# Optimization experiments

Hardware: AMD Instinct MI355X
Metric: run time of the kernel (lower is better)

Reference implementation:

```python
import jax, jax.numpy as jnp
import numpy as np

B, C, H, W = 16, 256, 112, 112
WS = 7           # window size
DH = 64          # dim_head
NH = C // DH     # num heads
EPS = 1e-5       # BatchNorm eps


def setup_inputs() -> dict:
    key = jax.random.key(0)
    ks = jax.random.split(key, 12)
    s = lambda k, shape, sc=0.05: jax.random.normal(k, shape, dtype=jnp.float32) * sc
    return dict(
        x_edge=jax.random.normal(ks[0], (B, C, H, W), dtype=jnp.float32),
        x_vit=jax.random.normal(ks[1], (B, C, H, W), dtype=jnp.float32),
        bn1_g=jnp.ones((C,), jnp.float32), bn1_b=jnp.zeros((C,), jnp.float32),
        bn1_m=s(ks[2], (C,)), bn1_v=jnp.abs(s(ks[3], (C,))) + 1.0,
        wq=s(ks[4], (C, C)), wk=s(ks[5], (C, C)), wv=s(ks[6], (C, C)),
        dw_w=s(ks[7], (C, 1, 3, 3)),
        bn2_g=jnp.ones((C,), jnp.float32), bn2_b=jnp.zeros((C,), jnp.float32),
        bn2_m=s(ks[8], (C,)), bn2_v=jnp.abs(s(ks[9], (C,))) + 1.0,
        eca_w=s(ks[10], (1, 1, 3)),
        wp=s(ks[11], (C, C)),
    )


def _bn(x, g, b, m, v):
    # eval-mode BatchNorm2d on NCHW
    scale = g * jax.lax.rsqrt(v + EPS)
    return (x - m[:, None, None]) * scale[:, None, None] + b[:, None, None]


def reference(x_edge, x_vit, bn1_g, bn1_b, bn1_m, bn1_v, wq, wk, wv, dw_w,
              bn2_g, bn2_b, bn2_m, bn2_v, eca_w, wp):
    x_fused = _bn(x_vit + x_edge, bn1_g, bn1_b, bn1_m, bn1_v)
    nh, nw = H // WS, W // WS  # H,W multiples of WS -> no padding needed

    def unfold(x):  # (B,C,H,W) -> (B*nh*nw, C, ws, ws)
        x = x.reshape(B, C, nh, WS, nw, WS).transpose(0, 2, 4, 1, 3, 5)
        return x.reshape(B * nh * nw, C, WS, WS)

    qw, kw, vw = unfold(x_edge), unfold(x_vit), unfold(x_fused)

    def heads(y):  # (N,C,ws,ws) -> (N, NH, ws*ws, DH)
        return y.reshape(-1, NH, DH, WS * WS).transpose(0, 1, 3, 2)

    q = heads(jnp.einsum('oc,ncij->noij', wq, qw))
    k = heads(jnp.einsum('oc,ncij->noij', wk, kw))
    v = heads(jax.nn.relu(jnp.einsum('oc,ncij->noij', wv, vw)))

    attn = jax.nn.softmax(jnp.einsum('nhqd,nhkd->nhqk', q, k) * (DH ** -0.5), axis=-1)
    x_sp = jnp.einsum('nhqk,nhkd->nhqd', attn, v)
    x_sp = x_sp.transpose(0, 1, 3, 2).reshape(-1, C, WS, WS)

    # importance-weighted blend with v_windows
    imp = jnp.abs(attn).mean(axis=(-1, -2)).mean(axis=1)  # (N,)
    imp = imp / (imp.max() + 1e-6)
    imp = imp[:, None, None, None]
    x_sp = imp * x_sp + (1.0 - imp) * vw

    # fold windows back to (B,C,H,W)
    x = x_sp.reshape(B, nh, nw, C, WS, WS).transpose(0, 3, 1, 4, 2, 5).reshape(B, C, H, W)

    # conv_local: depthwise 3x3 -> BN -> SiLU
    y = jax.lax.conv_general_dilated(x, dw_w, (1, 1), [(1, 1), (1, 1)],
                                     dimension_numbers=('NCHW', 'OIHW', 'NCHW'),
                                     feature_group_count=C)
    y = jax.nn.silu(_bn(y, bn2_g, bn2_b, bn2_m, bn2_v))

    # ECA: global avg pool -> conv1d over channels -> sigmoid gate
    p = y.mean(axis=(2, 3))[:, None, :]  # (B,1,C)
    a = jax.lax.conv_general_dilated(p, eca_w, (1,), [(1, 1)],
                                     dimension_numbers=('NCH', 'OIH', 'NCH'))
    y = y * jax.nn.sigmoid(a)[:, 0, :, None, None]

    # output 1x1 projection + skip
    y = jnp.einsum('oc,bcij->boij', wp, y)
    return x + y
```

## Files before the change

kernel.cpp:

```cpp
#include <hip/hip_runtime.h>

typedef unsigned short u16;
typedef __bf16 bf16x4 __attribute__((ext_vector_type(4)));
typedef __bf16 bf16x8 __attribute__((ext_vector_type(8)));
typedef float f32x4 __attribute__((ext_vector_type(4)));

#define MFMA_BF16(a, b, c) __builtin_amdgcn_mfma_f32_16x16x32_bf16((a), (b), (c), 0, 0, 0)
#define COMPILER_FENCE() asm volatile("" ::: "memory")

__device__ __forceinline__ bf16x8 ld_g16(const __bf16* p) {
  return *(const bf16x8*)p;
}
__device__ __forceinline__ bf16x8 ld_s16(const void* base, int byteoff) {
  return *(const bf16x8*)((const char*)base + byteoff);
}

__device__ __forceinline__ void proj_mfma(const __bf16* __restrict__ Wg,
                                          const __bf16* src, f32x4 (&acc)[4][4],
                                          int w, int lm, int lg)
{
  for (int ks = 0; ks < 8; ++ks) {
    bf16x8 afr[4], bfr[4];
#pragma unroll
    for (int mt = 0; mt < 4; ++mt)
      afr[mt] = ld_g16(Wg + (w * 64 + mt * 16 + lm) * 256 + ks * 32 + lg * 8);
#pragma unroll
    for (int nt = 0; nt < 4; ++nt) {
      int p = nt * 16 + lm;
      bfr[nt] = ld_s16(src, p * 512 + (((ks * 32 + lg * 8) * 2) ^ ((p & 7) << 4)));
    }
    __builtin_amdgcn_s_setprio(1);
#pragma unroll
    for (int mt = 0; mt < 4; ++mt)
#pragma unroll
      for (int nt = 0; nt < 4; ++nt)
        acc[mt][nt] = MFMA_BF16(afr[mt], bfr[nt], acc[mt][nt]);
    __builtin_amdgcn_s_setprio(0);
  }
}

__global__ void k0_setup(const float* __restrict__ wq, const float* __restrict__ wk,
                         const float* __restrict__ wv, const float* __restrict__ wp,
                         const float* __restrict__ g1, const float* __restrict__ b1,
                         const float* __restrict__ m1, const float* __restrict__ v1,
                         const float* __restrict__ g2, const float* __restrict__ b2,
                         const float* __restrict__ m2, const float* __restrict__ v2,
                         __bf16* __restrict__ wqb, __bf16* __restrict__ wkb,
                         __bf16* __restrict__ wvb, __bf16* __restrict__ wpb,
                         float* __restrict__ betav,
                         float* __restrict__ s2o, float* __restrict__ b2o)
{
  const int t = threadIdx.x;
  const int i = blockIdx.x * 256 + t;
  const int c = t;
  float s1 = g1[c] * rsqrtf(v1[c] + 1e-5f);
  wqb[i] = (__bf16)wq[i];
  wkb[i] = (__bf16)wk[i];
  wvb[i] = (__bf16)(wv[i] * s1);
  wpb[i] = (__bf16)wp[i];
  float contrib = wv[i] * (b1[c] - m1[c] * s1);
  contrib += __shfl_xor(contrib, 1);
  contrib += __shfl_xor(contrib, 2);
  contrib += __shfl_xor(contrib, 4);
  contrib += __shfl_xor(contrib, 8);
  contrib += __shfl_xor(contrib, 16);
  contrib += __shfl_xor(contrib, 32);
  __shared__ float rb[4];
  if ((t & 63) == 0) rb[t >> 6] = contrib;
  __syncthreads();
  if (t == 0) betav[blockIdx.x] = rb[0] + rb[1] + rb[2] + rb[3];
  if (blockIdx.x == 0) {
    float s2 = g2[t] * rsqrtf(v2[t] + 1e-5f);
    s2o[t] = s2;
    b2o[t] = b2[t] - m2[t] * s2;
  }
}

__global__ __launch_bounds__(256, 3) void k_pre(
    const float* __restrict__ xe, const float* __restrict__ xv,
    __bf16* __restrict__ tiles, int hb)
{
  __shared__ __align__(16) __bf16 st[32][788];
  const int t = threadIdx.x;
  const int blk = blockIdx.x;
  const int cg = blk & 7;
  const int wh = (blk >> 3) & 15;
  const int bl = blk >> 7;
  const int b = hb + bl;
  const int c0 = cg * 32;

  for (int s = 0; s < 2; ++s) {
    const float* src = (s == 0 ? xe : xv) + ((size_t)(b * 256 + c0) * 112 + wh * 7) * 112;
    for (int i = t; i < 6272; i += 256) {
      int cc = i / 196;
      int rem = i - cc * 196;
      f32x4 v = *(const f32x4*)(src + cc * 12544 + rem * 4);
      bf16x4 bv;
#pragma unroll
      for (int j = 0; j < 4; ++j) bv[j] = (__bf16)v[j];
      *(bf16x4*)&st[cc][rem * 4] = bv;
    }
    __syncthreads();
    for (int j = t; j < 3136; j += 256) {
      int row = j >> 2, sub = j & 3;
      int ww = row / 49, p = row - ww * 49;
      int y = p / 7, x = ww * 7 + (p - y * 7);
      int cs = sub * 8;
      bf16x8 v;
#pragma unroll
      for (int q = 0; q < 8; ++q) v[q] = st[cs + q][y * 112 + x];
      int n = (bl * 16 + wh) * 16 + ww;
      size_t off = (size_t)n * 50176 + s * 25088 + p * 512
                 + (((c0 + cs) * 2) ^ ((p & 7) << 4));
      *(bf16x8*)((char*)tiles + off) = v;
    }
    __syncthreads();
  }
}

__global__ __launch_bounds__(512, 4) void k1_attn(
    const __bf16* __restrict__ tiles,
    const __bf16* __restrict__ wqb, const __bf16* __restrict__ wkb,
    const __bf16* __restrict__ wvb, const float* __restrict__ betav,
    float* __restrict__ xout, int hb)
{
  __shared__ __align__(16) __bf16 B0[16384];
  __shared__ __align__(16) __bf16 B1[16384];

  const int t = threadIdx.x;
  const int n = blockIdx.x;
  const int bl = n >> 8, wh = (n >> 4) & 15, ww = n & 15;
  const int b = hb + bl;
  const int y0 = wh * 7, x0 = ww * 7;

  for (int idx = t; idx < 15 * 256; idx += 512) {
    int off = (49 + (idx >> 8)) * 512 + (idx & 255) * 2;
    *(__bf16*)((char*)B0 + off) = (__bf16)0.f;
    *(__bf16*)((char*)B1 + off) = (__bf16)0.f;
  }
  {
    const char* tb = (const char*)tiles + (size_t)n * 50176;
    for (int j = t; j < 3136; j += 512) {
      bf16x8 v = *(const bf16x8*)(tb + j * 16);
      char* d = (j < 1568) ? ((char*)B0 + j * 16) : ((char*)B1 + (j - 1568) * 16);
      *(bf16x8*)d = v;
    }
  }
  __syncthreads();

  const int w = t >> 6;
  const int l = t & 63;
  const int lm = l & 15, lg = l >> 4;
  const int h = w >> 1;
  const int half = w & 1;
  const int ob = w * 32;

  f32x4 vac[2][4] = {};
  {
    f32x4 qac[2][4] = {};
    for (int ks = 0; ks < 8; ++ks) {
      bf16x8 aq[2], av[2], bf[4];
#pragma unroll
      for (int mt = 0; mt < 2; ++mt) {
        int row = (ob + mt * 16 + lm) * 256 + ks * 32 + lg * 8;
        aq[mt] = ld_g16(wqb + row);
        av[mt] = ld_g16(wvb + row);
      }
#pragma unroll
      for (int nt = 0; nt < 4; ++nt) {
        int p = nt * 16 + lm;
        bf[nt] = ld_s16(B0, p * 512 + (((ks * 32 + lg * 8) * 2) ^ ((p & 7) << 4)));
      }
      __builtin_amdgcn_s_setprio(1);
#pragma unroll
      for (int mt = 0; mt < 2; ++mt)
#pragma unroll
        for (int nt = 0; nt < 4; ++nt) {
          qac[mt][nt] = MFMA_BF16(aq[mt], bf[nt], qac[mt][nt]);
          vac[mt][nt] = MFMA_BF16(av[mt], bf[nt], vac[mt][nt]);
        }
      __builtin_amdgcn_s_setprio(0);
    }
    __syncthreads();
#pragma unroll
    for (int mt = 0; mt < 2; ++mt)
#pragma unroll
      for (int nt = 0; nt < 4; ++nt) {
        int o0 = ob + mt * 16 + lg * 4;
        int p = nt * 16 + lm;
        bf16x4 v4;
#pragma unroll
        for (int r = 0; r < 4; ++r) v4[r] = (__bf16)qac[mt][nt][r];
        *(bf16x4*)((char*)B0 + p * 512 + ((o0 * 2) ^ ((p & 7) << 4))) = v4;
      }
  }

  {
    f32x4 kac[2][4] = {};
    for (int ks = 0; ks < 8; ++ks) {
      bf16x8 ak[2], av[2], bf[4];
#pragma unroll
      for (int mt = 0; mt < 2; ++mt) {
        int row = (ob + mt * 16 + lm) * 256 + ks * 32 + lg * 8;
        ak[mt] = ld_g16(wkb + row);
        av[mt] = ld_g16(wvb + row);
      }
#pragma unroll
      for (int nt = 0; nt < 4; ++nt) {
        int p = nt * 16 + lm;
        bf[nt] = ld_s16(B1, p * 512 + (((ks * 32 + lg * 8) * 2) ^ ((p & 7) << 4)));
      }
      __builtin_amdgcn_s_setprio(1);
#pragma unroll
      for (int mt = 0; mt < 2; ++mt)
#pragma unroll
        for (int nt = 0; nt < 4; ++nt) {
          kac[mt][nt] = MFMA_BF16(ak[mt], bf[nt], kac[mt][nt]);
          vac[mt][nt] = MFMA_BF16(av[mt], bf[nt], vac[mt][nt]);
        }
      __builtin_amdgcn_s_setprio(0);
    }
    __syncthreads();
#pragma unroll
    for (int mt = 0; mt < 2; ++mt)
#pragma unroll
      for (int nt = 0; nt < 4; ++nt) {
        int o0 = ob + mt * 16 + lg * 4;
        int p = nt * 16 + lm;
        bf16x4 v4;
#pragma unroll
        for (int r = 0; r < 4; ++r) v4[r] = (__bf16)kac[mt][nt][r];
        *(bf16x4*)((char*)B1 + p * 512 + ((o0 * 2) ^ ((p & 7) << 4))) = v4;
      }
  }
  __syncthreads();

  f32x4 sacc[2][4] = {};
  for (int ks = 0; ks < 2; ++ks) {
    bf16x8 aq[2], bk[4];
#pragma unroll
    for (int mt = 0; mt < 2; ++mt) {
      int qp = half * 32 + mt * 16 + lm;
      aq[mt] = ld_s16(B0, qp * 512 + (((h * 64 + ks * 32 + lg * 8) * 2) ^ ((qp & 7) << 4)));
    }
#pragma unroll
    for (int nt = 0; nt < 4; ++nt) {
      int kp = nt * 16 + lm;
      bk[nt] = ld_s16(B1, kp * 512 + (((h * 64 + ks * 32 + lg * 8) * 2) ^ ((kp & 7) << 4)));
    }
    __builtin_amdgcn_s_setprio(1);
#pragma unroll
    for (int mt = 0; mt < 2; ++mt)
#pragma unroll
      for (int nt = 0; nt < 4; ++nt)
        sacc[mt][nt] = MFMA_BF16(bk[nt], aq[mt], sacc[mt][nt]);
    __builtin_amdgcn_s_setprio(0);
  }

  COMPILER_FENCE();
#pragma unroll
  for (int mt = 0; mt < 2; ++mt) {
    float mx = -3.0e38f;
#pragma unroll
    for (int nt = 0; nt < 4; ++nt)
#pragma unroll
      for (int r = 0; r < 4; ++r) {
        float s = sacc[mt][nt][r] * 0.125f;
        sacc[mt][nt][r] = s;
        bool valid = (nt < 3) || (lg == 0 && r == 0);
        if (valid) mx = fmaxf(mx, s);
      }
    mx = fmaxf(mx, __shfl_xor(mx, 16));
    mx = fmaxf(mx, __shfl_xor(mx, 32));
    float sum = 0.f;
#pragma unroll
    for (int nt = 0; nt < 4; ++nt)
#pragma unroll
      for (int r = 0; r < 4; ++r) {
        bool valid = (nt < 3) || (lg == 0 && r == 0);
        float e = valid ? __expf(sacc[mt][nt][r] - mx) : 0.f;
        sacc[mt][nt][r] = e;
        sum += e;
      }
    sum += __shfl_xor(sum, 16);
    sum += __shfl_xor(sum, 32);
    float inv = 1.f / sum;
    int qp = half * 32 + mt * 16 + lm;
    int rowb = qp * 512 + h * 128;
    int sw = (qp & 7) << 4;
#pragma unroll
    for (int nt = 0; nt < 4; ++nt) {
      bf16x4 v4;
#pragma unroll
      for (int r = 0; r < 4; ++r) v4[r] = (__bf16)(sacc[mt][nt][r] * inv);
      int kp0 = nt * 16 + lg * 4;
      *(bf16x4*)((char*)B0 + rowb + ((kp0 * 2) ^ sw)) = v4;
    }
  }
  __syncthreads();

  {
    float beta[2][4];
#pragma unroll
    for (int mt = 0; mt < 2; ++mt) {
      f32x4 bv = *(const f32x4*)(betav + ob + mt * 16 + lg * 4);
#pragma unroll
      for (int r = 0; r < 4; ++r) beta[mt][r] = bv[r];
    }
#pragma unroll
    for (int mt = 0; mt < 2; ++mt)
#pragma unroll
      for (int nt = 0; nt < 4; ++nt)
#pragma unroll
        for (int r = 0; r < 4; ++r) {
          int o = ob + mt * 16 + lg * 4 + r;
          int kp = nt * 16 + lm;
          float val = fmaxf(vac[mt][nt][r] + beta[mt][r], 0.f);
          int off = o * 128 + ((kp * 2) ^ ((o & 7) << 4));
          *(__bf16*)((char*)B1 + off) = (__bf16)val;
        }
  }
  __syncthreads();

  f32x4 oacc[4][2] = {};
  for (int ks = 0; ks < 2; ++ks) {
    bf16x8 pf[2], bv[4];
#pragma unroll
    for (int mt = 0; mt < 2; ++mt) {
      int qp = half * 32 + mt * 16 + lm;
      pf[mt] = ld_s16(B0, qp * 512 + h * 128 + (((ks * 32 + lg * 8) * 2) ^ ((qp & 7) << 4)));
    }
#pragma unroll
    for (int nt = 0; nt < 4; ++nt) {
      int o = h * 64 + nt * 16 + lm;
      bv[nt] = ld_s16(B1, o * 128 + (((ks * 32 + lg * 8) * 2) ^ ((o & 7) << 4)));
    }
    __builtin_amdgcn_s_setprio(1);
#pragma unroll
    for (int nt = 0; nt < 4; ++nt)
#pragma unroll
      for (int mt = 0; mt < 2; ++mt)
        oacc[nt][mt] = MFMA_BF16(bv[nt], pf[mt], oacc[nt][mt]);
    __builtin_amdgcn_s_setprio(0);
  }

  const float IMP = (1.0f / 49.0f) / ((1.0f / 49.0f) + 1e-6f);
#pragma unroll
  for (int mt = 0; mt < 2; ++mt) {
    int qp = half * 32 + mt * 16 + lm;
    if (qp < 49) {
      int yy = y0 + qp / 7;
      int xx = x0 + qp % 7;
      size_t pix = (size_t)yy * 112 + xx;
#pragma unroll
      for (int nt = 0; nt < 4; ++nt)
#pragma unroll
        for (int r = 0; r < 4; ++r) {
          int o = h * 64 + nt * 16 + lg * 4 + r;
          xout[(size_t)(b * 256 + o) * 12544 + pix] = IMP * oacc[nt][mt][r];
        }
    }
  }
}

__global__ __launch_bounds__(256, 3) void k2_conv(
    const float* __restrict__ xin, const float* __restrict__ dww,
    const float* __restrict__ bn2s, const float* __restrict__ bn2b,
    __bf16* __restrict__ y1, float* __restrict__ pm)
{
  __shared__ __align__(16) float pl[12544];
  __shared__ float red[4];
  const int bc = blockIdx.x;
  const int c = bc & 255;
  const float* plane = xin + (size_t)bc * 12544;
  const int t = threadIdx.x;
  for (int i = t; i < 3136; i += 256)
    ((f32x4*)pl)[i] = ((const f32x4*)plane)[i];
  float wg[9];
#pragma unroll
  for (int i = 0; i < 9; ++i) wg[i] = dww[c * 9 + i];
  const float sc = bn2s[c], bi = bn2b[c];
  __syncthreads();

  const int x = t & 127;
  const int seg = t >> 7;
  float lsum = 0.f;
  if (x < 112) {
    const bool lok = x > 0, rok = x < 111;
    const int y0 = seg * 56;
    float m0, m1, m2, c0, c1, c2, p0, p1, p2;
    if (y0 == 0) {
      m0 = m1 = m2 = 0.f;
    } else {
      const float* rr = &pl[(y0 - 1) * 112 + x];
      m0 = lok ? rr[-1] : 0.f; m1 = rr[0]; m2 = rok ? rr[1] : 0.f;
    }
    {
      const float* rr = &pl[y0 * 112 + x];
      c0 = lok ? rr[-1] : 0.f; c1 = rr[0]; c2 = rok ? rr[1] : 0.f;
    }
#pragma unroll 4
    for (int y = y0; y < y0 + 56; ++y) {
      if (y < 111) {
        const float* rr = &pl[(y + 1) * 112 + x];
        p0 = lok ? rr[-1] : 0.f; p1 = rr[0]; p2 = rok ? rr[1] : 0.f;
      } else {
        p0 = p1 = p2 = 0.f;
      }
      float acc = m0 * wg[0] + m1 * wg[1] + m2 * wg[2]
                + c0 * wg[3] + c1 * wg[4] + c2 * wg[5]
                + p0 * wg[6] + p1 * wg[7] + p2 * wg[8];
      float u = acc * sc + bi;
      float sl = u / (1.f + __expf(-u));
      y1[(size_t)bc * 12544 + y * 112 + x] = (__bf16)sl;
      lsum += sl;
      m0 = c0; m1 = c1; m2 = c2;
      c0 = p0; c1 = p1; c2 = p2;
    }
  }
  lsum += __shfl_xor(lsum, 1);
  lsum += __shfl_xor(lsum, 2);
  lsum += __shfl_xor(lsum, 4);
  lsum += __shfl_xor(lsum, 8);
  lsum += __shfl_xor(lsum, 16);
  lsum += __shfl_xor(lsum, 32);
  if ((t & 63) == 0) red[t >> 6] = lsum;
  __syncthreads();
  if (t == 0) pm[bc] = (red[0] + red[1] + red[2] + red[3]) * (1.0f / 12544.0f);
}

__global__ void k3_eca(const float* __restrict__ pm, const float* __restrict__ ecaw,
                       float* __restrict__ gate)
{
  int b = blockIdx.x, c = threadIdx.x;
  float p0 = (c > 0) ? pm[b * 256 + c - 1] : 0.f;
  float p1 = pm[b * 256 + c];
  float p2 = (c < 255) ? pm[b * 256 + c + 1] : 0.f;
  float a = ecaw[0] * p0 + ecaw[1] * p1 + ecaw[2] * p2;
  gate[b * 256 + c] = 1.f / (1.f + __expf(-a));
}

__global__ __launch_bounds__(256, 3) void k4_out(
    const __bf16* __restrict__ y1, const float* __restrict__ gate,
    const __bf16* __restrict__ wpb, float* out_inout)
{
  __shared__ __align__(16) __bf16 bt[16384];
  const int t = threadIdx.x;
  const int blk = blockIdx.x;
  const int b = blk / 196;
  const int s0 = (blk - b * 196) * 64;
  const int chunk = t & 7, crow = t >> 3;
#pragma unroll
  for (int cc = 0; cc < 8; ++cc) {
    int c = cc * 32 + crow;
    float g = gate[b * 256 + c];
    const __bf16* src = y1 + (size_t)(b * 256 + c) * 12544 + s0 + chunk * 8;
    bf16x8 v = *(const bf16x8*)src;
#pragma unroll
    for (int j = 0; j < 8; ++j) {
      int s = chunk * 8 + j;
      float f = (float)v[j] * g;
      *(__bf16*)((char*)bt + s * 512 + ((c * 2) ^ ((s & 7) << 4))) = (__bf16)f;
    }
  }
  __syncthreads();
  const int w = t >> 6, l = t & 63, lm = l & 15, lg = l >> 4;
  f32x4 acc[4][4] = {};
  proj_mfma(wpb, bt, acc, w, lm, lg);
#pragma unroll
  for (int mt = 0; mt < 4; ++mt)
#pragma unroll
    for (int nt = 0; nt < 4; ++nt)
#pragma unroll
      for (int r = 0; r < 4; ++r) {
        int o = w * 64 + mt * 16 + lg * 4 + r;
        int s = nt * 16 + lm;
        size_t idx = (size_t)(b * 256 + o) * 12544 + s0 + s;
        out_inout[idx] = out_inout[idx] + acc[mt][nt][r];
      }
}

extern "C" void kernel_launch(void* const* d_in, const int* in_sizes, int n_in,
                              void* d_out, int out_size, void* d_ws, size_t ws_size,
                              hipStream_t stream) {
  const float* x_edge = (const float*)d_in[0];
  const float* x_vit  = (const float*)d_in[1];
  const float* bn1_g  = (const float*)d_in[2];
  const float* bn1_b  = (const float*)d_in[3];
  const float* bn1_m  = (const float*)d_in[4];
  const float* bn1_v  = (const float*)d_in[5];
  const float* wq     = (const float*)d_in[6];
  const float* wk     = (const float*)d_in[7];
  const float* wv     = (const float*)d_in[8];
  const float* dw_w   = (const float*)d_in[9];
  const float* bn2_g  = (const float*)d_in[10];
  const float* bn2_b  = (const float*)d_in[11];
  const float* bn2_m  = (const float*)d_in[12];
  const float* bn2_v  = (const float*)d_in[13];
  const float* eca_w  = (const float*)d_in[14];
  const float* wp     = (const float*)d_in[15];

  float* out = (float*)d_out;

  char* ws = (char*)d_ws;
  __bf16* tiles = (__bf16*)ws;
  __bf16* y1    = (__bf16*)ws;
  const size_t o1 = 102760448;
  __bf16* wqb  = (__bf16*)(ws + o1);
  __bf16* wkb  = (__bf16*)(ws + o1 + 131072);
  __bf16* wvb  = (__bf16*)(ws + o1 + 262144);
  __bf16* wpb  = (__bf16*)(ws + o1 + 393216);
  float*  betav= (float*)(ws + o1 + 524288);
  float*  bn2s = (float*)(ws + o1 + 525312);
  float*  bn2bb= (float*)(ws + o1 + 526336);
  float*  pm   = (float*)(ws + o1 + 527360);
  float*  gate = (float*)(ws + o1 + 543744);

  hipLaunchKernelGGL(k0_setup, dim3(256), dim3(256), 0, stream,
                     wq, wk, wv, wp, bn1_g, bn1_b, bn1_m, bn1_v,
                     bn2_g, bn2_b, bn2_m, bn2_v,
                     wqb, wkb, wvb, wpb, betav, bn2s, bn2bb);
  for (int hb = 0; hb < 16; hb += 8) {
    hipLaunchKernelGGL(k_pre, dim3(1024), dim3(256), 0, stream,
                       x_edge, x_vit, tiles, hb);
    hipLaunchKernelGGL(k1_attn, dim3(2048), dim3(512), 0, stream,
                       tiles, wqb, wkb, wvb, betav, out, hb);
  }
  hipLaunchKernelGGL(k2_conv, dim3(4096), dim3(256), 0, stream,
                     out, dw_w, bn2s, bn2bb, y1, pm);
  hipLaunchKernelGGL(k3_eca, dim3(16), dim3(256), 0, stream, pm, eca_w, gate);
  hipLaunchKernelGGL(k4_out, dim3(3136), dim3(256), 0, stream,
                     y1, gate, wpb, out);
}
```

Before: 784.8 us.

## Restructure attention LDS into three regions to cut barriers and zero-fill

```diff
diff --git a/kernel.cpp b/kernel.cpp
--- a/kernel.cpp
+++ b/kernel.cpp
@@ -124,8 +124,10 @@
     const __bf16* __restrict__ wvb, const float* __restrict__ betav,
     float* __restrict__ xout, int hb)
 {
-  __shared__ __align__(16) __bf16 B0[16384];
-  __shared__ __align__(16) __bf16 B1[16384];
+  __shared__ __align__(16) char LDSB[78912];
+  char* RXE = LDSB;
+  char* RQ  = LDSB + 25088;
+  char* RV  = LDSB + 50176;
 
   const int t = threadIdx.x;
   const int n = blockIdx.x;
@@ -133,17 +135,16 @@
   const int b = hb + bl;
   const int y0 = wh * 7, x0 = ww * 7;
 
-  for (int idx = t; idx < 15 * 256; idx += 512) {
-    int off = (49 + (idx >> 8)) * 512 + (idx & 255) * 2;
-    *(__bf16*)((char*)B0 + off) = (__bf16)0.f;
-    *(__bf16*)((char*)B1 + off) = (__bf16)0.f;
-  }
   {
     const char* tb = (const char*)tiles + (size_t)n * 50176;
     for (int j = t; j < 3136; j += 512) {
       bf16x8 v = *(const bf16x8*)(tb + j * 16);
-      char* d = (j < 1568) ? ((char*)B0 + j * 16) : ((char*)B1 + (j - 1568) * 16);
+      char* d = (j < 1568) ? (RXE + j * 16) : (RV + (j - 1568) * 16);
       *(bf16x8*)d = v;
+    }
+    if (t < 4) {
+      bf16x8 z = {};
+      *(bf16x8*)(RV + 28672 + t * 16) = z;
     }
   }
   __syncthreads();
@@ -169,7 +170,7 @@
 #pragma unroll
       for (int nt = 0; nt < 4; ++nt) {
         int p = nt * 16 + lm;
-        bf[nt] = ld_s16(B0, p * 512 + (((ks * 32 + lg * 8) * 2) ^ ((p & 7) << 4)));
+        bf[nt] = ld_s16(RXE, p * 512 + (((ks * 32 + lg * 8) * 2) ^ ((p & 7) << 4)));
       }
       __builtin_amdgcn_s_setprio(1);
 #pragma unroll
@@ -181,57 +182,82 @@
         }
       __builtin_amdgcn_s_setprio(0);
     }
-    __syncthreads();
 #pragma unroll
     for (int mt = 0; mt < 2; ++mt)
-#pragma unroll
-      for (int nt = 0; nt < 4; ++nt) {
-        int o0 = ob + mt * 16 + lg * 4;
-        int p = nt * 16 + lm;
-        bf16x4 v4;
-#pragma unroll
-        for (int r = 0; r < 4; ++r) v4[r] = (__bf16)qac[mt][nt][r];
-        *(bf16x4*)((char*)B0 + p * 512 + ((o0 * 2) ^ ((p & 7) << 4))) = v4;
-      }
-  }
-
-  {
-    f32x4 kac[2][4] = {};
-    for (int ks = 0; ks < 8; ++ks) {
-      bf16x8 ak[2], av[2], bf[4];
-#pragma unroll
-      for (int mt = 0; mt < 2; ++mt) {
-        int row = (ob + mt * 16 + lm) * 256 + ks * 32 + lg * 8;
-        ak[mt] = ld_g16(wkb + row);
-        av[mt] = ld_g16(wvb + row);
-      }
 #pragma unroll
       for (int nt = 0; nt < 4; ++nt) {
         int p = nt * 16 + lm;
-        bf[nt] = ld_s16(B1, p * 512 + (((ks * 32 + lg * 8) * 2) ^ ((p & 7) << 4)));
-      }
-      __builtin_amdgcn_s_setprio(1);
-#pragma unroll
-      for (int mt = 0; mt < 2; ++mt)
-#pragma unroll
-        for (int nt = 0; nt < 4; ++nt) {
-          kac[mt][nt] = MFMA_BF16(ak[mt], bf[nt], kac[mt][nt]);
-          vac[mt][nt] = MFMA_BF16(av[mt], bf[nt], vac[mt][nt]);
+        if (nt < 3 || lm == 0) {
+          int o0 = ob + mt * 16 + lg * 4;
+          bf16x4 v4;
+#pragma unroll
+          for (int r = 0; r < 4; ++r) v4[r] = (__bf16)qac[mt][nt][r];
+          *(bf16x4*)(RQ + p * 512 + ((o0 * 2) ^ ((p & 7) << 4))) = v4;
         }
-      __builtin_amdgcn_s_setprio(0);
-    }
-    __syncthreads();
+      }
+  }
+
+  f32x4 kac[2][4] = {};
+  for (int ks = 0; ks < 8; ++ks) {
+    bf16x8 ak[2], av[2], bf[4];
+#pragma unroll
+    for (int mt = 0; mt < 2; ++mt) {
+      int row = (ob + mt * 16 + lm) * 256 + ks * 32 + lg * 8;
+      ak[mt] = ld_g16(wkb + row);
+      av[mt] = ld_g16(wvb + row);
+    }
+#pragma unroll
+    for (int nt = 0; nt < 4; ++nt) {
+      int p = nt * 16 + lm;
+      bf[nt] = ld_s16(RV, p * 512 + (((ks * 32 + lg * 8) * 2) ^ ((p & 7) << 4)));
+    }
+    __builtin_amdgcn_s_setprio(1);
 #pragma unroll
     for (int mt = 0; mt < 2; ++mt)
 #pragma unroll
       for (int nt = 0; nt < 4; ++nt) {
+        kac[mt][nt] = MFMA_BF16(ak[mt], bf[nt], kac[mt][nt]);
+        vac[mt][nt] = MFMA_BF16(av[mt], bf[nt], vac[mt][nt]);
+      }
+    __builtin_amdgcn_s_setprio(0);
+  }
+  __syncthreads();
+
+#pragma unroll
+  for (int mt = 0; mt < 2; ++mt)
+#pragma unroll
+    for (int nt = 0; nt < 4; ++nt) {
+      int p = nt * 16 + lm;
+      if (nt < 3 || lm == 0) {
         int o0 = ob + mt * 16 + lg * 4;
-        int p = nt * 16 + lm;
         bf16x4 v4;
 #pragma unroll
         for (int r = 0; r < 4; ++r) v4[r] = (__bf16)kac[mt][nt][r];
-        *(bf16x4*)((char*)B1 + p * 512 + ((o0 * 2) ^ ((p & 7) << 4))) = v4;
-      }
+        *(bf16x4*)(RXE + p * 512 + ((o0 * 2) ^ ((p & 7) << 4))) = v4;
+      }
+    }
+
+  {
+    float beta[2][4];
+#pragma unroll
+    for (int mt = 0; mt < 2; ++mt) {
+      f32x4 bv = *(const f32x4*)(betav + ob + mt * 16 + lg * 4);
+#pragma unroll
+      for (int r = 0; r < 4; ++r) beta[mt][r] = bv[r];
+    }
+#pragma unroll
+    for (int mt = 0; mt < 2; ++mt)
+#pragma unroll
+      for (int nt = 0; nt < 4; ++nt)
+#pragma unroll
+        for (int r = 0; r < 4; ++r) {
+          int kp = nt * 16 + lm;
+          if (nt < 3 || lm < 8) {
+            int o = ob + mt * 16 + lg * 4 + r;
+            float val = fminf(fmaxf(vac[mt][nt][r] + beta[mt][r], 0.f), 1e30f);
+            *(__bf16*)(RV + o * 112 + kp * 2) = (__bf16)val;
+          }
+        }
   }
   __syncthreads();
 
@@ -241,12 +267,12 @@
 #pragma unroll
     for (int mt = 0; mt < 2; ++mt) {
       int qp = half * 32 + mt * 16 + lm;
-      aq[mt] = ld_s16(B0, qp * 512 + (((h * 64 + ks * 32 + lg * 8) * 2) ^ ((qp & 7) << 4)));
+      aq[mt] = ld_s16(RQ, qp * 512 + (((h * 64 + ks * 32 + lg * 8) * 2) ^ ((qp & 7) << 4)));
     }
 #pragma unroll
     for (int nt = 0; nt < 4; ++nt) {
       int kp = nt * 16 + lm;
-      bk[nt] = ld_s16(B1, kp * 512 + (((h * 64 + ks * 32 + lg * 8) * 2) ^ ((kp & 7) << 4)));
+      bk[nt] = ld_s16(RXE, kp * 512 + (((h * 64 + ks * 32 + lg * 8) * 2) ^ ((kp & 7) << 4)));
     }
     __builtin_amdgcn_s_setprio(1);
 #pragma unroll
@@ -286,41 +312,20 @@
     sum += __shfl_xor(sum, 32);
     float inv = 1.f / sum;
     int qp = half * 32 + mt * 16 + lm;
-    int rowb = qp * 512 + h * 128;
-    int sw = (qp & 7) << 4;
-#pragma unroll
-    for (int nt = 0; nt < 4; ++nt) {
-      bf16x4 v4;
-#pragma unroll
-      for (int r = 0; r < 4; ++r) v4[r] = (__bf16)(sacc[mt][nt][r] * inv);
-      int kp0 = nt * 16 + lg * 4;
-      *(bf16x4*)((char*)B0 + rowb + ((kp0 * 2) ^ sw)) = v4;
-    }
-  }
-  __syncthreads();
-
-  {
-    float beta[2][4];
-#pragma unroll
-    for (int mt = 0; mt < 2; ++mt) {
-      f32x4 bv = *(const f32x4*)(betav + ob + mt * 16 + lg * 4);
-#pragma unroll
-      for (int r = 0; r < 4; ++r) beta[mt][r] = bv[r];
-    }
-#pragma unroll
-    for (int mt = 0; mt < 2; ++mt)
-#pragma unroll
-      for (int nt = 0; nt < 4; ++nt)
-#pragma unroll
-        for (int r = 0; r < 4; ++r) {
-          int o = ob + mt * 16 + lg * 4 + r;
-          int kp = nt * 16 + lm;
-          float val = fmaxf(vac[mt][nt][r] + beta[mt][r], 0.f);
-          int off = o * 128 + ((kp * 2) ^ ((o & 7) << 4));
-          *(__bf16*)((char*)B1 + off) = (__bf16)val;
-        }
-  }
-  __syncthreads();
+    if (qp < 49) {
+      int rowb = qp * 512 + h * 128;
+      int sw = (qp & 7) << 4;
+#pragma unroll
+      for (int nt = 0; nt < 4; ++nt) {
+        bf16x4 v4;
+#pragma unroll
+        for (int r = 0; r < 4; ++r) v4[r] = (__bf16)(sacc[mt][nt][r] * inv);
+        int kp0 = nt * 16 + lg * 4;
+        *(bf16x4*)(RQ + rowb + ((kp0 * 2) ^ sw)) = v4;
+      }
+    }
+  }
+  COMPILER_FENCE();
 
   f32x4 oacc[4][2] = {};
   for (int ks = 0; ks < 2; ++ks) {
@@ -328,12 +333,12 @@
 #pragma unroll
     for (int mt = 0; mt < 2; ++mt) {
       int qp = half * 32 + mt * 16 + lm;
-      pf[mt] = ld_s16(B0, qp * 512 + h * 128 + (((ks * 32 + lg * 8) * 2) ^ ((qp & 7) << 4)));
+      pf[mt] = ld_s16(RQ, qp * 512 + h * 128 + (((ks * 32 + lg * 8) * 2) ^ ((qp & 7) << 4)));
     }
 #pragma unroll
     for (int nt = 0; nt < 4; ++nt) {
       int o = h * 64 + nt * 16 + lm;
-      bv[nt] = ld_s16(B1, o * 128 + (((ks * 32 + lg * 8) * 2) ^ ((o & 7) << 4)));
+      bv[nt] = ld_s16(RV, o * 112 + (ks * 32 + lg * 8) * 2);
     }
     __builtin_amdgcn_s_setprio(1);
 #pragma unroll
```

New measurement: 881.6 us. 12.3% more time.
